# Optimization experiments

Hardware: AMD Instinct MI355X
Metric: run time of the kernel (lower is better)

The kernel has to match this reference:

```python
import jax, jax.numpy as jnp
import numpy as np

BATCH, HIDDEN, DIM_X, N_FORCING, DIM_T, MODES = 16, 128, 128, 4, 64, 96


def setup_inputs() -> dict:
    key = jax.random.key(0)
    k1, k2, k3, k4, k5 = jax.random.split(key, 5)
    scale = 1.0 / HIDDEN ** 2
    return {
        "z0": jax.random.normal(k1, (BATCH, HIDDEN, DIM_X), jnp.float32),
        "xi": jax.random.normal(k2, (BATCH, N_FORCING, DIM_X, DIM_T), jnp.float32),
        "A": scale * jax.random.uniform(k3, (2, MODES, HIDDEN, HIDDEN), jnp.float32),
        "W_F": jax.random.normal(k4, (HIDDEN, HIDDEN), jnp.float32) / np.sqrt(HIDDEN).astype(np.float32),
        "W_G": jax.random.normal(k5, (HIDDEN, N_FORCING, HIDDEN), jnp.float32) / np.sqrt(HIDDEN).astype(np.float32),
    }


def _spde_func(z, W_F, W_G):
    # z: (b, h, x) -> F_z: (b, h, x), G_z: (b, h, n, x)
    F_z = jnp.tanh(jnp.einsum('oh,bhx->box', W_F, z))
    G_z = jnp.tanh(jnp.einsum('onh,bhx->bonx', W_G, z))
    return F_z, G_z


def _compl_mat_vec_mul_1d(A, z):
    # A: (2, modes, h, h); z: (batch, 2, modes, h) -- (real, imag) stacked on dim 1
    op = lambda M, u: jnp.einsum('xij,bxj->bxi', M, u)
    re = op(A[0], z[:, 0]) - op(A[1], z[:, 1])
    im = op(A[1], z[:, 0]) - op(A[0], z[:, 1])  # faithful to original (minus sign)
    return jnp.stack([re, im], axis=1)


def _prod(v, xi_t, A, W_F, W_G, a, b):
    # v: (batch, 2, dim_x, hidden); xi_t: (batch, dim_x, n_forcing) = dX/dt at step i
    Av = jnp.zeros_like(v).at[:, :, a:b].set(_compl_mat_vec_mul_1d(A, v[:, :, a:b]))
    vc = v[:, 0] + 1j * v[:, 1]                      # (b, x, h) complex
    z = jnp.fft.ifft(jnp.fft.ifftshift(vc, axes=1), axis=1).real  # (b, x, h)
    z = jnp.transpose(z, (0, 2, 1))                  # (b, h, x)
    F_z, G_z = _spde_func(z, W_F, W_G)
    G_z_xi = jnp.einsum('bhnx,bxn->bhx', G_z, xi_t)
    H = F_z + G_z_xi                                 # (b, h, x)
    hf = jnp.fft.fftshift(jnp.fft.fft(H, axis=2), axes=2)
    hf = jnp.stack([hf.real, hf.imag], axis=1)       # (b, 2, h, x)
    hf = jnp.transpose(hf, (0, 1, 3, 2))             # (b, 2, x, h)
    out_ft = jnp.zeros_like(v).at[:, :, a:b].set(hf[:, :, a:b])
    return Av + out_ft


def reference(z0, xi, A, W_F, W_G):
    batch, hidden, dim_x = z0.shape
    modes = A.shape[1]
    a, b = dim_x // 2 - modes // 2, dim_x // 2 + modes // 2
    # v0: band-limited shifted FFT of z0, layout (b, 2, x, h)
    z0_ft = jnp.fft.fftshift(jnp.fft.fft(z0, axis=2), axes=2)
    z0_ft = jnp.stack([z0_ft.real, z0_ft.imag], axis=1)            # (b, 2, h, x)
    v0 = jnp.zeros_like(z0_ft).at[:, :, :, a:b].set(z0_ft[:, :, :, a:b])
    v0 = jnp.transpose(v0, (0, 1, 3, 2))                           # (b, 2, x, h)
    # control increments: linear interp slope on uniform grid t=arange(T), dt=1
    xi_path = jnp.transpose(xi, (0, 2, 3, 1))                      # (b, x, t, n)
    dxi = xi_path[:, :, 1:, :] - xi_path[:, :, :-1, :]             # (b, x, t-1, n)
    dxi = jnp.moveaxis(dxi, 2, 0)                                  # (t-1, b, x, n)

    def step(v, d):
        v_new = v + _prod(v, d, A, W_F, W_G, a, b)  # Euler, dt = 1
        return v_new, v_new

    _, traj = jax.lax.scan(step, v0, dxi)                          # (t-1, b, 2, x, h)
    traj = jnp.concatenate([v0[None], traj], axis=0)               # (t, b, 2, x, h)
    vc = traj[:, :, 0] + 1j * traj[:, :, 1]                        # (t, b, x, h)
    vc = jnp.transpose(vc, (1, 3, 2, 0))                           # (b, h, x, t)
    z = jnp.fft.ifft(jnp.fft.ifftshift(vc, axes=2), axis=2).real   # (b, h, x, t)
    return z
```

## Files before the change

### kernel.cpp

```cpp
#include <hip/hip_runtime.h>
#include <math.h>

#define BATCH 16
#define HID   128
#define NX    128
#define NF    4
#define NT    64
#define MODES 96
#define OM    (5 * HID)
#define NWG   256
#define TPB   1024
#define GSZ   16
#define ZSZ   ((size_t)BATCH * NX * HID)

__global__ void k_tables(float* __restrict__ C, float* __restrict__ S,
                         float2* __restrict__ T2m) {
    int m = blockIdx.x, x = threadIdx.x;
    if (x < NX) {
        int k = (80 + m) % NX;
        float ang = (float)((k * x) & (NX - 1)) * (2.0f * (float)M_PI / (float)NX);
        float c = cosf(ang), s = sinf(ang);
        C[m * NX + x] = c;
        S[m * NX + x] = s;
        T2m[m * NX + x] = make_float2(c, s);
    }
}

__global__ void k_dxi(const float* __restrict__ xi, float* __restrict__ dxi) {
    int idx = blockIdx.x * blockDim.x + threadIdx.x;
    const int total = (NT - 1) * BATCH * NX * NF;
    if (idx < total) {
        int n = idx & (NF - 1);
        int x = (idx >> 2) & (NX - 1);
        int b = (idx >> 9) & (BATCH - 1);
        int t = idx >> 13;
        const float* base = xi + (((size_t)b * NF + n) * NX + x) * NT;
        dxi[idx] = base[t + 1] - base[t];
    }
}

__global__ void k_wt(const float* __restrict__ WF, const float* __restrict__ WG,
                     float* __restrict__ Wt) {
    __shared__ float t[32][33];
    int g = blockIdx.z;
    int h0 = blockIdx.x * 32, o0 = blockIdx.y * 32;
    int tx = threadIdx.x, ty = threadIdx.y;
    #pragma unroll
    for (int j = 0; j < 32; j += 8) {
        int o = o0 + ty + j;
        t[ty + j][tx] = (g == 0) ? WF[(size_t)o * HID + h0 + tx]
                                 : WG[((size_t)o * NF + (g - 1)) * HID + h0 + tx];
    }
    __syncthreads();
    #pragma unroll
    for (int j = 0; j < 32; j += 8)
        Wt[(size_t)(h0 + ty + j) * OM + g * HID + o0 + tx] = t[tx][ty + j];
}

__global__ void k_at2(const float* __restrict__ A, float2* __restrict__ At2) {
    __shared__ float t0[32][33], t1[32][33];
    int m = blockIdx.z;
    int h0 = blockIdx.x * 32, o0 = blockIdx.y * 32;
    int tx = threadIdx.x, ty = threadIdx.y;
    const float* A0 = A + (size_t)m * HID * HID;
    const float* A1 = A0 + (size_t)MODES * HID * HID;
    #pragma unroll
    for (int j = 0; j < 32; j += 8) {
        t0[ty + j][tx] = A0[(size_t)(o0 + ty + j) * HID + h0 + tx];
        t1[ty + j][tx] = A1[(size_t)(o0 + ty + j) * HID + h0 + tx];
    }
    __syncthreads();
    #pragma unroll
    for (int j = 0; j < 32; j += 8)
        At2[((size_t)m * HID + h0 + ty + j) * HID + o0 + tx] =
            make_float2(t0[tx][ty + j], t1[tx][ty + j]);
}

__global__ __launch_bounds__(TPB, 1) void k_solve(
    const float* __restrict__ z0, const float* __restrict__ Ct,
    const float* __restrict__ St, const float2* __restrict__ T2m,
    const float* __restrict__ Wt, const float2* __restrict__ At2,
    const float* __restrict__ dxi, float* __restrict__ va,
    float* __restrict__ vb, float* __restrict__ zbuf,
    float* __restrict__ out, int* __restrict__ barc)
{
    __shared__ float Csh[MODES][8];
    __shared__ float Ssh[MODES][8];
    __shared__ float zsl[HID][129];
    __shared__ float Wsl[HID][41];
    __shared__ float Hcl[NX][9];
    __shared__ float dxs[NX][NF];

    const int w = blockIdx.x;
    const int t = threadIdx.x;
    const int grp = w >> 4;
    const int j = w & 15;
    const int b = grp;
    const int xg0 = j * 8;
    const int o0 = j * 8;

    int nbar = 0;
    int* ctr = barc + grp * 64;
    auto gbar = [&]() {
        ++nbar;
        __syncthreads();
        if (t == 0) {
            __hip_atomic_fetch_add(ctr, 1, __ATOMIC_RELEASE,
                                   __HIP_MEMORY_SCOPE_AGENT);
            while (__hip_atomic_load(ctr, __ATOMIC_RELAXED,
                                     __HIP_MEMORY_SCOPE_AGENT) < GSZ * nbar)
                __builtin_amdgcn_s_sleep(2);
            (void)__hip_atomic_load(ctr, __ATOMIC_ACQUIRE,
                                    __HIP_MEMORY_SCOPE_AGENT);
        }
        __syncthreads();
    };

    if (t < MODES * 8) {
        int m = t >> 3, xp = t & 7;
        Csh[m][xp] = Ct[m * NX + xg0 + xp];
        Ssh[m][xp] = St[m * NX + xg0 + xp];
    }

    {
        int h = t & 127, q = t >> 7;
        int c = q & 1, mq = q >> 1;
        const float* zr = z0 + ((size_t)b * HID + h) * NX;
        #pragma unroll
        for (int jj = 0; jj < 2; ++jj) {
            int mm = mq + 4 * jj;
            if (mm < 6) {
                int m = j * 6 + mm;
                const float* Trow = (c ? St : Ct) + m * NX;
                float acc = 0.f;
                #pragma unroll 4
                for (int x = 0; x < NX; ++x) acc += zr[x] * Trow[x];
                if (c) acc = -acc;
                va[(((size_t)b * 2 + c) * MODES + m) * HID + h] = acc;
            }
        }
    }
    gbar();

    float* vcur = va;
    float* vnxt = vb;

    for (int step = 0; step < NT; ++step) {
        if (step > 0 && (step & 15) == 0) {
            int t0 = step - 16;
            int xl = t >> 7, h = t & 127;
            int x = xg0 + xl;
            float vals[16];
            #pragma unroll
            for (int tt = 0; tt < 16; ++tt)
                vals[tt] = zbuf[(size_t)tt * ZSZ + ((size_t)b * NX + x) * HID + h];
            float* dst = out + (((size_t)b * HID + h) * NX + x) * NT + t0;
            #pragma unroll
            for (int q = 0; q < 4; ++q)
                ((float4*)dst)[q] = make_float4(vals[q*4], vals[q*4+1],
                                                vals[q*4+2], vals[q*4+3]);
        }

        {
            int h = t & 127, xp = t >> 7;
            const float* vr = vcur + ((size_t)b * 2) * MODES * HID + h;
            const float* vi = vr + (size_t)MODES * HID;
            float acc = 0.f;
            #pragma unroll 4
            for (int m = 0; m < MODES; ++m) {
                acc += vr[m * HID] * Csh[m][xp] - vi[m * HID] * Ssh[m][xp];
            }
            acc *= 0.0078125f;
            zbuf[(size_t)(step & 15) * ZSZ + ((size_t)b * NX + xg0 + xp) * HID + h] = acc;
        }
        if (step == NT - 1) break;
        gbar();

        {
            const float4* z4 = (const float4*)(zbuf + (size_t)(step & 15) * ZSZ
                                               + (size_t)b * NX * HID);
            #pragma unroll
            for (int k = 0; k < 4; ++k) {
                float4 v4 = z4[t + k * 1024];
                int idx = (t + k * 1024) * 4;
                int x = idx >> 7, h = idx & 127;
                zsl[h][x] = v4.x; zsl[h + 1][x] = v4.y;
                zsl[h + 2][x] = v4.z; zsl[h + 3][x] = v4.w;
            }
            #pragma unroll
            for (int k = 0; k < 5; ++k) {
                int idx = t + k * 1024;
                int h = idx / 40, col = idx - h * 40;
                int g = col >> 3, ol = col & 7;
                Wsl[h][col] = Wt[(size_t)h * OM + g * HID + o0 + ol];
            }
            if (t < 512)
                dxs[t >> 2][t & 3] =
                    dxi[((size_t)step * BATCH + b) * NX * NF + t];
            __syncthreads();

            int ol = t & 7, x = t >> 3;
            float acc[5] = {0, 0, 0, 0, 0};
            #pragma unroll 4
            for (int h = 0; h < HID; ++h) {
                float zv = zsl[h][x];
                #pragma unroll
                for (int g = 0; g < 5; ++g)
                    acc[g] += Wsl[h][g * 8 + ol] * zv;
            }
            float hv = tanhf(acc[0])
                     + tanhf(acc[1]) * dxs[x][0]
                     + tanhf(acc[2]) * dxs[x][1]
                     + tanhf(acc[3]) * dxs[x][2]
                     + tanhf(acc[4]) * dxs[x][3];
            Hcl[x][ol] = hv;
            __syncthreads();
        }

        if (t < 768) {
            int ol = t & 7, m = t >> 3;
            int o = o0 + ol;
            float fre = 0.f, fim = 0.f;
            #pragma unroll 4
            for (int x = 0; x < NX; ++x) {
                float hv = Hcl[x][ol];
                float2 ts = T2m[(size_t)m * NX + x];
                fre += hv * ts.x;
                fim -= hv * ts.y;
            }
            const float2* a2 = At2 + ((size_t)m * HID) * HID + o;
            const float* vr = vcur + (((size_t)b * 2 + 0) * MODES + m) * HID;
            const float* vi = vcur + (((size_t)b * 2 + 1) * MODES + m) * HID;
            float are = 0.f, aim = 0.f;
            #pragma unroll 4
            for (int h = 0; h < HID; ++h) {
                float2 a = a2[(size_t)h * HID];
                float r = vr[h], i2 = vi[h];
                are += a.x * r - a.y * i2;
                aim += a.y * r - a.x * i2;
            }
            vnxt[(((size_t)b * 2 + 0) * MODES + m) * HID + o] = vr[o] + are + fre;
            vnxt[(((size_t)b * 2 + 1) * MODES + m) * HID + o] = vi[o] + aim + fim;
        }
        gbar();

        float* tmp = vcur; vcur = vnxt; vnxt = tmp;
    }

    {
        int xl = t >> 7, h = t & 127;
        int x = xg0 + xl;
        float vals[16];
        #pragma unroll
        for (int tt = 0; tt < 16; ++tt)
            vals[tt] = zbuf[(size_t)tt * ZSZ + ((size_t)b * NX + x) * HID + h];
        float* dst = out + (((size_t)b * HID + h) * NX + x) * NT + 48;
        #pragma unroll
        for (int q = 0; q < 4; ++q)
            ((float4*)dst)[q] = make_float4(vals[q*4], vals[q*4+1],
                                            vals[q*4+2], vals[q*4+3]);
    }
}

extern "C" void kernel_launch(void* const* d_in, const int* in_sizes, int n_in,
                              void* d_out, int out_size, void* d_ws, size_t ws_size,
                              hipStream_t stream) {
    const float* z0 = (const float*)d_in[0];
    const float* xi = (const float*)d_in[1];
    const float* A  = (const float*)d_in[2];
    const float* WF = (const float*)d_in[3];
    const float* WG = (const float*)d_in[4];
    float* out = (float*)d_out;

    float* ws = (float*)d_ws;
    size_t off = 0;
    auto alloc = [&](size_t n) { float* p = ws + off; off += n; return p; };

    float*  Ct   = alloc((size_t)MODES * NX);
    float*  St   = alloc((size_t)MODES * NX);
    float2* T2m  = (float2*)alloc((size_t)MODES * NX * 2);
    float*  Wt   = alloc((size_t)HID * OM);
    float2* At2  = (float2*)alloc((size_t)MODES * HID * HID * 2);
    float*  va   = alloc((size_t)BATCH * 2 * MODES * HID);
    float*  vb   = alloc((size_t)BATCH * 2 * MODES * HID);
    float*  dxib = alloc((size_t)(NT - 1) * BATCH * NX * NF);
    float*  zbuf = alloc(16 * ZSZ);
    int*    barc = (int*)alloc(BATCH * 64);

    hipMemsetAsync(barc, 0, BATCH * 64 * sizeof(int), stream);
    k_tables<<<MODES, 128, 0, stream>>>(Ct, St, T2m);
    {
        int total = (NT - 1) * BATCH * NX * NF;
        k_dxi<<<(total + 255) / 256, 256, 0, stream>>>(xi, dxib);
    }
    k_wt<<<dim3(4, 4, 5), dim3(32, 8), 0, stream>>>(WF, WG, Wt);
    k_at2<<<dim3(4, 4, MODES), dim3(32, 8), 0, stream>>>(A, At2);

    k_solve<<<NWG, TPB, 0, stream>>>(z0, Ct, St, T2m, Wt, At2, dxib,
                                     va, vb, zbuf, out, barc);
}
```

Measured before the change: 4.159 ms.

## Interleave complex state, preload weights once, repartition spectral update by modes

The spectral state is stored as interleaved float2 (real, imag), and each workgroup's slice of the F/G weights is packed into float4 plus float layouts and loaded into shared memory once, before the time loop. Before, those weights were reloaded on every step. The z tile is now stored x-major with vectorized writes. The H result goes to global memory, and an extra grid barrier lets each workgroup own 6 modes across all 128 outputs rather than 8 outputs across all modes. This cuts per-step weight traffic and repeated DFT work, at the cost of an additional grid-wide barrier and a global round trip for H on each step.

```diff
diff --git a/kernel.cpp b/kernel.cpp
--- a/kernel.cpp
+++ b/kernel.cpp
@@ -7,7 +7,6 @@
 #define NF    4
 #define NT    64
 #define MODES 96
-#define OM    (5 * HID)
 #define NWG   256
 #define TPB   1024
 #define GSZ   16
@@ -39,22 +38,18 @@
     }
 }
 
-__global__ void k_wt(const float* __restrict__ WF, const float* __restrict__ WG,
-                     float* __restrict__ Wt) {
-    __shared__ float t[32][33];
-    int g = blockIdx.z;
-    int h0 = blockIdx.x * 32, o0 = blockIdx.y * 32;
-    int tx = threadIdx.x, ty = threadIdx.y;
-    #pragma unroll
-    for (int j = 0; j < 32; j += 8) {
-        int o = o0 + ty + j;
-        t[ty + j][tx] = (g == 0) ? WF[(size_t)o * HID + h0 + tx]
-                                 : WG[((size_t)o * NF + (g - 1)) * HID + h0 + tx];
-    }
-    __syncthreads();
-    #pragma unroll
-    for (int j = 0; j < 32; j += 8)
-        Wt[(size_t)(h0 + ty + j) * OM + g * HID + o0 + tx] = t[tx][ty + j];
+__global__ void k_wt4(const float* __restrict__ WF, const float* __restrict__ WGm,
+                      float4* __restrict__ Wt4, float* __restrict__ Wt1) {
+    int idx = blockIdx.x * 256 + threadIdx.x;
+    if (idx < 16 * HID * 8) {
+        int ol = idx & 7, h = (idx >> 3) & 127, j = idx >> 10;
+        int o = j * 8 + ol;
+        Wt4[idx] = make_float4(WF[(size_t)o * HID + h],
+                               WGm[((size_t)o * NF + 0) * HID + h],
+                               WGm[((size_t)o * NF + 1) * HID + h],
+                               WGm[((size_t)o * NF + 2) * HID + h]);
+        Wt1[idx] = WGm[((size_t)o * NF + 3) * HID + h];
+    }
 }
 
 __global__ void k_at2(const float* __restrict__ A, float2* __restrict__ At2) {
@@ -79,28 +74,29 @@
 __global__ __launch_bounds__(TPB, 1) void k_solve(
     const float* __restrict__ z0, const float* __restrict__ Ct,
     const float* __restrict__ St, const float2* __restrict__ T2m,
-    const float* __restrict__ Wt, const float2* __restrict__ At2,
-    const float* __restrict__ dxi, float* __restrict__ va,
-    float* __restrict__ vb, float* __restrict__ zbuf,
+    const float4* __restrict__ Wt4g, const float* __restrict__ Wt1g,
+    const float2* __restrict__ At2, const float* __restrict__ dxi,
+    float2* __restrict__ va, float2* __restrict__ vb,
+    float* __restrict__ zbuf, float* __restrict__ Hc,
     float* __restrict__ out, int* __restrict__ barc)
 {
-    __shared__ float Csh[MODES][8];
-    __shared__ float Ssh[MODES][8];
-    __shared__ float zsl[HID][129];
-    __shared__ float Wsl[HID][41];
-    __shared__ float Hcl[NX][9];
-    __shared__ float dxs[NX][NF];
+    __shared__ float2 CS[MODES][8];
+    __shared__ float  zsl[NX][132];
+    __shared__ float4 Wsl4[HID][8];
+    __shared__ float  Wsl1[HID][9];
+    __shared__ float  dxs[NX][5];
+    __shared__ float2 vsl[6][HID];
 
     const int w = blockIdx.x;
     const int t = threadIdx.x;
-    const int grp = w >> 4;
+    const int b = w >> 4;
     const int j = w & 15;
-    const int b = grp;
     const int xg0 = j * 8;
     const int o0 = j * 8;
+    const int m0 = j * 6;
 
     int nbar = 0;
-    int* ctr = barc + grp * 64;
+    int* ctr = barc + b * 64;
     auto gbar = [&]() {
         ++nbar;
         __syncthreads();
@@ -118,32 +114,37 @@
 
     if (t < MODES * 8) {
         int m = t >> 3, xp = t & 7;
-        Csh[m][xp] = Ct[m * NX + xg0 + xp];
-        Ssh[m][xp] = St[m * NX + xg0 + xp];
+        CS[m][xp] = T2m[m * NX + xg0 + xp];
+    }
+    {
+        int h = t >> 3, ol = t & 7;
+        Wsl4[h][ol] = Wt4g[((size_t)j * HID + h) * 8 + ol];
+        Wsl1[h][ol] = Wt1g[((size_t)j * HID + h) * 8 + ol];
     }
 
     {
         int h = t & 127, q = t >> 7;
         int c = q & 1, mq = q >> 1;
         const float* zr = z0 + ((size_t)b * HID + h) * NX;
+        float* fva = (float*)va;
         #pragma unroll
         for (int jj = 0; jj < 2; ++jj) {
             int mm = mq + 4 * jj;
             if (mm < 6) {
-                int m = j * 6 + mm;
+                int m = m0 + mm;
                 const float* Trow = (c ? St : Ct) + m * NX;
                 float acc = 0.f;
                 #pragma unroll 4
                 for (int x = 0; x < NX; ++x) acc += zr[x] * Trow[x];
                 if (c) acc = -acc;
-                va[(((size_t)b * 2 + c) * MODES + m) * HID + h] = acc;
+                fva[(((size_t)b * MODES + m) * HID + h) * 2 + c] = acc;
             }
         }
     }
     gbar();
 
-    float* vcur = va;
-    float* vnxt = vb;
+    float2* vcur = va;
+    float2* vnxt = vb;
 
     for (int step = 0; step < NT; ++step) {
         if (step > 0 && (step & 15) == 0) {
@@ -163,12 +164,13 @@
 
         {
             int h = t & 127, xp = t >> 7;
-            const float* vr = vcur + ((size_t)b * 2) * MODES * HID + h;
-            const float* vi = vr + (size_t)MODES * HID;
+            const float2* vr = vcur + (size_t)b * MODES * HID + h;
             float acc = 0.f;
             #pragma unroll 4
             for (int m = 0; m < MODES; ++m) {
-                acc += vr[m * HID] * Csh[m][xp] - vi[m * HID] * Ssh[m][xp];
+                float2 vv = vr[(size_t)m * HID];
+                float2 cs = CS[m][xp];
+                acc += vv.x * cs.x - vv.y * cs.y;
             }
             acc *= 0.0078125f;
             zbuf[(size_t)(step & 15) * ZSZ + ((size_t)b * NX + xg0 + xp) * HID + h] = acc;
@@ -181,18 +183,9 @@
                                                + (size_t)b * NX * HID);
             #pragma unroll
             for (int k = 0; k < 4; ++k) {
-                float4 v4 = z4[t + k * 1024];
-                int idx = (t + k * 1024) * 4;
-                int x = idx >> 7, h = idx & 127;
-                zsl[h][x] = v4.x; zsl[h + 1][x] = v4.y;
-                zsl[h + 2][x] = v4.z; zsl[h + 3][x] = v4.w;
-            }
-            #pragma unroll
-            for (int k = 0; k < 5; ++k) {
                 int idx = t + k * 1024;
-                int h = idx / 40, col = idx - h * 40;
-                int g = col >> 3, ol = col & 7;
-                Wsl[h][col] = Wt[(size_t)h * OM + g * HID + o0 + ol];
+                int x = idx >> 5, h4 = (idx & 31) * 4;
+                *(float4*)&zsl[x][h4] = z4[idx];
             }
             if (t < 512)
                 dxs[t >> 2][t & 3] =
@@ -200,51 +193,63 @@
             __syncthreads();
 
             int ol = t & 7, x = t >> 3;
-            float acc[5] = {0, 0, 0, 0, 0};
+            float a0 = 0.f, a1 = 0.f, a2 = 0.f, a3 = 0.f, a4 = 0.f;
             #pragma unroll 4
             for (int h = 0; h < HID; ++h) {
-                float zv = zsl[h][x];
-                #pragma unroll
-                for (int g = 0; g < 5; ++g)
-                    acc[g] += Wsl[h][g * 8 + ol] * zv;
-            }
-            float hv = tanhf(acc[0])
-                     + tanhf(acc[1]) * dxs[x][0]
-                     + tanhf(acc[2]) * dxs[x][1]
-                     + tanhf(acc[3]) * dxs[x][2]
-                     + tanhf(acc[4]) * dxs[x][3];
-            Hcl[x][ol] = hv;
+                float zv = zsl[x][h];
+                float4 w4 = Wsl4[h][ol];
+                float w1 = Wsl1[h][ol];
+                a0 += w4.x * zv; a1 += w4.y * zv;
+                a2 += w4.z * zv; a3 += w4.w * zv;
+                a4 += w1 * zv;
+            }
+            float hv = tanhf(a0)
+                     + tanhf(a1) * dxs[x][0]
+                     + tanhf(a2) * dxs[x][1]
+                     + tanhf(a3) * dxs[x][2]
+                     + tanhf(a4) * dxs[x][3];
+            Hc[((size_t)b * NX + x) * HID + o0 + ol] = hv;
             __syncthreads();
         }
-
-        if (t < 768) {
-            int ol = t & 7, m = t >> 3;
-            int o = o0 + ol;
-            float fre = 0.f, fim = 0.f;
-            #pragma unroll 4
-            for (int x = 0; x < NX; ++x) {
-                float hv = Hcl[x][ol];
-                float2 ts = T2m[(size_t)m * NX + x];
-                fre += hv * ts.x;
-                fim -= hv * ts.y;
-            }
-            const float2* a2 = At2 + ((size_t)m * HID) * HID + o;
-            const float* vr = vcur + (((size_t)b * 2 + 0) * MODES + m) * HID;
-            const float* vi = vcur + (((size_t)b * 2 + 1) * MODES + m) * HID;
-            float are = 0.f, aim = 0.f;
-            #pragma unroll 4
-            for (int h = 0; h < HID; ++h) {
-                float2 a = a2[(size_t)h * HID];
-                float r = vr[h], i2 = vi[h];
-                are += a.x * r - a.y * i2;
-                aim += a.y * r - a.x * i2;
-            }
-            vnxt[(((size_t)b * 2 + 0) * MODES + m) * HID + o] = vr[o] + are + fre;
-            vnxt[(((size_t)b * 2 + 1) * MODES + m) * HID + o] = vi[o] + aim + fim;
-        }
         gbar();
 
-        float* tmp = vcur; vcur = vnxt; vnxt = tmp;
+        {
+            if (t < 6 * HID) {
+                int ml = t >> 7, h = t & 127;
+                vsl[ml][h] = vcur[((size_t)b * MODES + m0 + ml) * HID + h];
+            }
+            __syncthreads();
+            if (t < 768) {
+                int o = t & 127, ml = t >> 7;
+                int m = m0 + ml;
+                const float* hp = Hc + (size_t)b * NX * HID + o;
+                const float2* trow = T2m + (size_t)m * NX;
+                float fre = 0.f, fim = 0.f;
+                #pragma unroll 4
+                for (int x = 0; x < NX; ++x) {
+                    float hv = hp[(size_t)x * HID];
+                    float2 cs = trow[x];
+                    fre += hv * cs.x;
+                    fim -= hv * cs.y;
+                }
+                const float2* a2p = At2 + ((size_t)m * HID) * HID + o;
+                float are = 0.f, aim = 0.f;
+                #pragma unroll 4
+                for (int h = 0; h < HID; ++h) {
+                    float2 a = a2p[(size_t)h * HID];
+                    float2 vv = vsl[ml][h];
+                    are += a.x * vv.x - a.y * vv.y;
+                    aim += a.y * vv.x - a.x * vv.y;
+                }
+                float2 vo = vsl[ml][o];
+                vnxt[((size_t)b * MODES + m) * HID + o] =
+                    make_float2(vo.x + are + fre, vo.y + aim + fim);
+            }
+            __syncthreads();
+        }
+        gbar();
+
+        float2* tmp = vcur; vcur = vnxt; vnxt = tmp;
     }
 
     {
@@ -279,10 +284,12 @@
     float*  Ct   = alloc((size_t)MODES * NX);
     float*  St   = alloc((size_t)MODES * NX);
     float2* T2m  = (float2*)alloc((size_t)MODES * NX * 2);
-    float*  Wt   = alloc((size_t)HID * OM);
+    float4* Wt4  = (float4*)alloc((size_t)16 * HID * 8 * 4);
+    float*  Wt1  = alloc((size_t)16 * HID * 8);
     float2* At2  = (float2*)alloc((size_t)MODES * HID * HID * 2);
-    float*  va   = alloc((size_t)BATCH * 2 * MODES * HID);
-    float*  vb   = alloc((size_t)BATCH * 2 * MODES * HID);
+    float2* va   = (float2*)alloc((size_t)BATCH * MODES * HID * 2);
+    float2* vb   = (float2*)alloc((size_t)BATCH * MODES * HID * 2);
+    float*  Hcb  = alloc((size_t)BATCH * NX * HID);
     float*  dxib = alloc((size_t)(NT - 1) * BATCH * NX * NF);
     float*  zbuf = alloc(16 * ZSZ);
     int*    barc = (int*)alloc(BATCH * 64);
@@ -293,9 +300,9 @@
         int total = (NT - 1) * BATCH * NX * NF;
         k_dxi<<<(total + 255) / 256, 256, 0, stream>>>(xi, dxib);
     }
-    k_wt<<<dim3(4, 4, 5), dim3(32, 8), 0, stream>>>(WF, WG, Wt);
+    k_wt4<<<64, 256, 0, stream>>>(WF, WG, Wt4, Wt1);
     k_at2<<<dim3(4, 4, MODES), dim3(32, 8), 0, stream>>>(A, At2);
 
-    k_solve<<<NWG, TPB, 0, stream>>>(z0, Ct, St, T2m, Wt, At2, dxib,
-                                     va, vb, zbuf, out, barc);
-}
+    k_solve<<<NWG, TPB, 0, stream>>>(z0, Ct, St, T2m, Wt4, Wt1, At2, dxib,
+                                     va, vb, zbuf, Hcb, out, barc);
+}
```

Result: faster. 3.805 ms (-8.5%).
